# Kernel tuning notes

Measured on AMD Instinct MI355X. Metric: run time of the kernel, lower is better.

The kernel has to match this reference:

```python
import jax, jax.numpy as jnp
import numpy as np

D_IN = 1024
D_OUT = 1024
SEQ = 2048
BATCH = 4


def setup_inputs() -> dict:
    key = jax.random.key(0)
    kx, kq, kk, kv = jax.random.split(key, 4)
    x = jax.random.normal(kx, (BATCH, SEQ, D_IN), dtype=jnp.float32)
    s = 1.0 / np.sqrt(D_IN)
    Wq = jax.random.uniform(kq, (D_IN, D_OUT), dtype=jnp.float32, minval=-s, maxval=s)
    Wk = jax.random.uniform(kk, (D_IN, D_OUT), dtype=jnp.float32, minval=-s, maxval=s)
    Wv = jax.random.uniform(kv, (D_IN, D_OUT), dtype=jnp.float32, minval=-s, maxval=s)
    return {"x": x, "Wq": Wq, "Wk": Wk, "Wv": Wv}


def reference(x, Wq, Wk, Wv):
    d_k = Wq.shape[1]
    q = jnp.einsum('bsd,de->bse', x, Wq)
    k = jnp.einsum('bsd,de->bse', x, Wk)
    v = jnp.einsum('bsd,de->bse', x, Wv)
    # [B, S, S] raw scores
    scores = jnp.einsum('bqe,bke->bqk', q, k)
    S = scores.shape[-1]
    causal = jnp.triu(jnp.ones((S, S), dtype=bool), k=1)  # True above diagonal
    scores = jnp.where(causal, -jnp.inf, scores)
    attn = jax.nn.softmax(scores * (d_k ** -0.5), axis=-1)
    # dropout p=0.0 -> identity
    return jnp.einsum('bqk,bke->bqe', attn, v)
```

## Files before the change

kernel.cpp:

```cpp
#include <hip/hip_runtime.h>
#include <hip/hip_bf16.h>

typedef unsigned short u16;
typedef __bf16 bfx8 __attribute__((ext_vector_type(8)));
typedef float fx4 __attribute__((ext_vector_type(4)));

#define SEQ 2048
#define DIM 1024
#define NBATCH 4
#define SCALE 0.03125f
#define NEL ((size_t)NBATCH * SEQ * DIM)

__device__ inline u16 f2bf(float f) {
    __bf16 h = (__bf16)f;
    return __builtin_bit_cast(unsigned short, h);
}

#define GLL(gp, lp) __builtin_amdgcn_global_load_lds( \
    (const __attribute__((address_space(1))) unsigned int*)(gp), \
    (__attribute__((address_space(3))) unsigned int*)(lp), 16, 0, 0)

__global__ __launch_bounds__(256) void prep(
    const float* __restrict__ X,
    const float* __restrict__ Wq, const float* __restrict__ Wk,
    const float* __restrict__ Wv,
    u16* __restrict__ XB, u16* __restrict__ WB, u16* __restrict__ WTv,
    float* __restrict__ Lrow)
{
    __shared__ u16 t[32][33];
    int bid = blockIdx.x;
    int tid = threadIdx.x;
    if (bid < 8192) {
        size_t i = (size_t)bid * 256 + tid;
        float4 v = ((const float4*)X)[i];
        uint2 pk;
        pk.x = (unsigned)f2bf(v.x) | ((unsigned)f2bf(v.y) << 16);
        pk.y = (unsigned)f2bf(v.z) | ((unsigned)f2bf(v.w) << 16);
        ((uint2*)XB)[i] = pk;
    } else if (bid < 10240) {
        int b2 = bid - 8192;
        const float* W = (b2 < 1024) ? Wq : Wk;
        u16* out = WB + (size_t)(b2 >> 10) * 1024 * 1024;
        size_t i = (size_t)(b2 & 1023) * 256 + tid;
        float4 v = ((const float4*)W)[i];
        uint2 pk;
        pk.x = (unsigned)f2bf(v.x) | ((unsigned)f2bf(v.y) << 16);
        pk.y = (unsigned)f2bf(v.z) | ((unsigned)f2bf(v.w) << 16);
        ((uint2*)out)[i] = pk;
    } else if (bid < 11264) {
        int t2 = bid - 10240;
        int n0 = (t2 & 31) * 32, k0 = (t2 >> 5) * 32;
        int tx = tid & 31, ty = tid >> 5;
        #pragma unroll
        for (int i = 0; i < 32; i += 8)
            t[ty + i][tx] = f2bf(Wv[(size_t)(k0 + ty + i) * 1024 + n0 + tx]);
        __syncthreads();
        #pragma unroll
        for (int i = 0; i < 32; i += 8)
            WTv[(size_t)(n0 + ty + i) * 1024 + k0 + tx] = t[tx][ty + i];
    } else {
        int i = (bid - 11264) * 256 + tid;
        Lrow[i] = 0.0f;
    }
}

__global__ __launch_bounds__(256) void gemm_m(
    const u16* __restrict__ WBk, const u16* __restrict__ WBq, u16* __restrict__ MT)
{
    int m0 = blockIdx.y * 128, n0 = blockIdx.x * 128;
    __shared__ __align__(16) u16 As[128 * 32];
    __shared__ __align__(16) u16 Bs[128 * 32];
    int tid = threadIdx.x, lane = tid & 63, w = tid >> 6;
    int wm = w >> 1, wn = w & 1, lo = lane & 15, qd = lane >> 4;
    fx4 acc[4][4] = {};

    int c0 = tid, c1 = tid + 256;
    const u16* a0 = WBk + (size_t)(m0 + (c0 >> 2)) * 1024 + (((c0 & 3) ^ ((c0 >> 2) & 3)) * 8);
    const u16* a1 = WBk + (size_t)(m0 + (c1 >> 2)) * 1024 + (((c1 & 3) ^ ((c1 >> 2) & 3)) * 8);
    const u16* b0 = WBq + (size_t)(n0 + (c0 >> 2)) * 1024 + (((c0 & 3) ^ ((c0 >> 2) & 3)) * 8);
    const u16* b1 = WBq + (size_t)(n0 + (c1 >> 2)) * 1024 + (((c1 & 3) ^ ((c1 >> 2) & 3)) * 8);

    int sw = (qd ^ (lo & 3)) * 8;
    for (int k0 = 0; k0 < 1024; k0 += 32) {
        GLL(a0 + k0, &As[(size_t)c0 * 8]);
        GLL(a1 + k0, &As[(size_t)c1 * 8]);
        GLL(b0 + k0, &Bs[(size_t)c0 * 8]);
        GLL(b1 + k0, &Bs[(size_t)c1 * 8]);
        __syncthreads();
        bfx8 af[4], bf[4];
        #pragma unroll
        for (int i = 0; i < 4; i++)
            af[i] = *(const bfx8*)(&As[(wm * 64 + i * 16 + lo) * 32 + sw]);
        #pragma unroll
        for (int j = 0; j < 4; j++)
            bf[j] = *(const bfx8*)(&Bs[(wn * 64 + j * 16 + lo) * 32 + sw]);
        #pragma unroll
        for (int i = 0; i < 4; i++)
            #pragma unroll
            for (int j = 0; j < 4; j++)
                acc[i][j] = __builtin_amdgcn_mfma_f32_16x16x32_bf16(af[i], bf[j], acc[i][j], 0, 0, 0);
        __syncthreads();
    }
    #pragma unroll
    for (int i = 0; i < 4; i++)
        #pragma unroll
        for (int j = 0; j < 4; j++)
            #pragma unroll
            for (int r = 0; r < 4; r++)
                MT[(size_t)(m0 + wm * 64 + i * 16 + qd * 4 + r) * 1024
                   + n0 + wn * 64 + j * 16 + lo] = f2bf(acc[i][j][r]);
}

__global__ __launch_bounds__(256) void gemm_fast(
    const u16* __restrict__ XB, const u16* __restrict__ MT,
    const u16* __restrict__ WTv,
    u16* __restrict__ Yo, u16* __restrict__ VTo)
{
    const u16* Wz = (blockIdx.z == 0) ? MT : WTv;
    int m0 = blockIdx.y * 128, n0 = blockIdx.x * 128;

    __shared__ __align__(16) u16 As[128 * 32];
    __shared__ __align__(16) u16 Bs[128 * 32];
    __shared__ __align__(16) u16 Ct[64][132];

    int tid = threadIdx.x, lane = tid & 63, w = tid >> 6;
    int wm = w >> 1, wn = w & 1, lo = lane & 15, qd = lane >> 4;

    fx4 acc[4][4] = {};

    int c0 = tid, c1 = tid + 256;
    const u16* a0 = XB + (size_t)(m0 + (c0 >> 2)) * 1024 + (((c0 & 3) ^ ((c0 >> 2) & 3)) * 8);
    const u16* a1 = XB + (size_t)(m0 + (c1 >> 2)) * 1024 + (((c1 & 3) ^ ((c1 >> 2) & 3)) * 8);
    const u16* b0 = Wz + (size_t)(n0 + (c0 >> 2)) * 1024 + (((c0 & 3) ^ ((c0 >> 2) & 3)) * 8);
    const u16* b1 = Wz + (size_t)(n0 + (c1 >> 2)) * 1024 + (((c1 & 3) ^ ((c1 >> 2) & 3)) * 8);

    int sw = (qd ^ (lo & 3)) * 8;
    for (int k0 = 0; k0 < 1024; k0 += 32) {
        GLL(a0 + k0, &As[(size_t)c0 * 8]);
        GLL(a1 + k0, &As[(size_t)c1 * 8]);
        GLL(b0 + k0, &Bs[(size_t)c0 * 8]);
        GLL(b1 + k0, &Bs[(size_t)c1 * 8]);
        __syncthreads();

        bfx8 af[4], bf[4];
        #pragma unroll
        for (int i = 0; i < 4; i++)
            af[i] = *(const bfx8*)(&As[(wm * 64 + i * 16 + lo) * 32 + sw]);
        #pragma unroll
        for (int j = 0; j < 4; j++)
            bf[j] = *(const bfx8*)(&Bs[(wn * 64 + j * 16 + lo) * 32 + sw]);
        #pragma unroll
        for (int i = 0; i < 4; i++)
            #pragma unroll
            for (int j = 0; j < 4; j++)
                acc[i][j] = __builtin_amdgcn_mfma_f32_16x16x32_bf16(af[i], bf[j], acc[i][j], 0, 0, 0);
        __syncthreads();
    }

    if (blockIdx.z == 0) {
        #pragma unroll
        for (int i = 0; i < 4; i++)
            #pragma unroll
            for (int j = 0; j < 4; j++)
                #pragma unroll
                for (int r = 0; r < 4; r++) {
                    int row = m0 + wm * 64 + i * 16 + qd * 4 + r;
                    int col = n0 + wn * 64 + j * 16 + lo;
                    Yo[(size_t)row * 1024 + col] = f2bf(acc[i][j][r]);
                }
    } else {
        #pragma unroll
        for (int half = 0; half < 2; half++) {
            __syncthreads();
            if (wm == half) {
                #pragma unroll
                for (int i = 0; i < 4; i++)
                    #pragma unroll
                    for (int j = 0; j < 4; j++)
                        #pragma unroll
                        for (int r = 0; r < 4; r++)
                            Ct[i * 16 + qd * 4 + r][wn * 64 + j * 16 + lo] = f2bf(acc[i][j][r]);
            }
            __syncthreads();
            #pragma unroll
            for (int e = tid; e < 64 * 128; e += 256) {
                int d = e >> 6, sl = e & 63;
                int gr = m0 + half * 64 + sl;
                int bb = gr >> 11, s = gr & 2047;
                VTo[((size_t)bb * DIM + (n0 + d)) * SEQ + s] = Ct[sl][d];
            }
        }
    }
}

__global__ __launch_bounds__(512) void sgemm_exp(
    const u16* __restrict__ Y, const u16* __restrict__ XB,
    u16* __restrict__ P, float* __restrict__ Lrow)
{
    int b = blockIdx.y;
    int t = blockIdx.x;
    int i = (int)((sqrtf(8.0f * t + 1.0f) - 1.0f) * 0.5f);
    while ((i + 1) * (i + 2) / 2 <= t) i++;
    while (i * (i + 1) / 2 > t) i--;
    int j = t - i * (i + 1) / 2;

    const u16* Yb = Y + (size_t)b * SEQ * DIM;
    const u16* Xb = XB + (size_t)b * SEQ * DIM;
    u16* Pb = P + (size_t)b * SEQ * SEQ;
    float* Lb = Lrow + (size_t)b * SEQ;

    int m0 = i * 128, n0 = j * 128;

    __shared__ __align__(16) u16 As[128 * 64];
    __shared__ __align__(16) u16 Bs[128 * 64];

    int tid = threadIdx.x, lane = tid & 63, w = tid >> 6;
    int wm = w >> 2, wn = w & 3, lo = lane & 15, qd = lane >> 4;

    fx4 acc[4][2] = {};

    int c0 = tid, c1 = tid + 512;
    const u16* a0 = Yb + (size_t)(m0 + (c0 >> 3)) * 1024 + (((c0 & 7) ^ ((c0 >> 3) & 7)) * 8);
    const u16* a1 = Yb + (size_t)(m0 + (c1 >> 3)) * 1024 + (((c1 & 7) ^ ((c1 >> 3) & 7)) * 8);
    const u16* b0 = Xb + (size_t)(n0 + (c0 >> 3)) * 1024 + (((c0 & 7) ^ ((c0 >> 3) & 7)) * 8);
    const u16* b1 = Xb + (size_t)(n0 + (c1 >> 3)) * 1024 + (((c1 & 7) ^ ((c1 >> 3) & 7)) * 8);

    for (int k0 = 0; k0 < 1024; k0 += 64) {
        GLL(a0 + k0, &As[(size_t)c0 * 8]);
        GLL(a1 + k0, &As[(size_t)c1 * 8]);
        GLL(b0 + k0, &Bs[(size_t)c0 * 8]);
        GLL(b1 + k0, &Bs[(size_t)c1 * 8]);
        __syncthreads();

        #pragma unroll
        for (int kc = 0; kc < 2; kc++) {
            int sw = ((kc * 4 + qd) ^ (lo & 7)) * 8;
            bfx8 af[4], bf[2];
            #pragma unroll
            for (int ii = 0; ii < 4; ii++)
                af[ii] = *(const bfx8*)(&As[(wm * 64 + ii * 16 + lo) * 64 + sw]);
            #pragma unroll
            for (int jn = 0; jn < 2; jn++)
                bf[jn] = *(const bfx8*)(&Bs[(wn * 32 + jn * 16 + lo) * 64 + sw]);
            #pragma unroll
            for (int ii = 0; ii < 4; ii++)
                #pragma unroll
                for (int jn = 0; jn < 2; jn++)
                    acc[ii][jn] = __builtin_amdgcn_mfma_f32_16x16x32_bf16(af[ii], bf[jn], acc[ii][jn], 0, 0, 0);
        }
        __syncthreads();
    }

    #pragma unroll
    for (int ii = 0; ii < 4; ii++)
        #pragma unroll
        for (int r = 0; r < 4; r++) {
            int row = m0 + wm * 64 + ii * 16 + qd * 4 + r;
            float rs = 0.0f;
            #pragma unroll
            for (int jn = 0; jn < 2; jn++) {
                int col = n0 + wn * 32 + jn * 16 + lo;
                float s = acc[ii][jn][r] * SCALE;
                s = fminf(fmaxf(s, -30.0f), 30.0f);
                float p = (col > row) ? 0.0f : __expf(s);
                Pb[(size_t)row * SEQ + col] = f2bf(p);
                rs += p;
            }
            #pragma unroll
            for (int off = 1; off < 16; off <<= 1) rs += __shfl_xor(rs, off);
            if (lo == 0) atomicAdd(&Lb[row], rs);
        }
}

__global__ __launch_bounds__(512) void pvgemm(
    const u16* __restrict__ P, const u16* __restrict__ VT,
    const float* __restrict__ Lrow, float* __restrict__ O)
{
    int b = blockIdx.y;
    int qb = 15 - (int)(blockIdx.x >> 3);
    int db = blockIdx.x & 7;
    int m0 = qb * 128, n0 = db * 128;
    int kext = (qb + 1) * 128;

    const u16* Pb = P + (size_t)b * SEQ * SEQ;
    const u16* Vb = VT + (size_t)b * DIM * SEQ;
    const float* Lb = Lrow + (size_t)b * SEQ;
    float* Ob = O + (size_t)b * SEQ * DIM;

    __shared__ __align__(16) u16 As[128 * 64];
    __shared__ __align__(16) u16 Bs[128 * 64];

    int tid = threadIdx.x, lane = tid & 63, w = tid >> 6;
    int wm = w >> 2, wn = w & 3, lo = lane & 15, qd = lane >> 4;

    fx4 acc[4][2] = {};

    int c0 = tid, c1 = tid + 512;
    const u16* a0 = Pb + (size_t)(m0 + (c0 >> 3)) * SEQ + (((c0 & 7) ^ ((c0 >> 3) & 7)) * 8);
    const u16* a1 = Pb + (size_t)(m0 + (c1 >> 3)) * SEQ + (((c1 & 7) ^ ((c1 >> 3) & 7)) * 8);
    const u16* b0 = Vb + (size_t)(n0 + (c0 >> 3)) * SEQ + (((c0 & 7) ^ ((c0 >> 3) & 7)) * 8);
    const u16* b1 = Vb + (size_t)(n0 + (c1 >> 3)) * SEQ + (((c1 & 7) ^ ((c1 >> 3) & 7)) * 8);

    for (int k0 = 0; k0 < kext; k0 += 64) {
        GLL(a0 + k0, &As[(size_t)c0 * 8]);
        GLL(a1 + k0, &As[(size_t)c1 * 8]);
        GLL(b0 + k0, &Bs[(size_t)c0 * 8]);
        GLL(b1 + k0, &Bs[(size_t)c1 * 8]);
        __syncthreads();

        #pragma unroll
        for (int kc = 0; kc < 2; kc++) {
            int sw = ((kc * 4 + qd) ^ (lo & 7)) * 8;
            bfx8 af[4], bf[2];
            #pragma unroll
            for (int ii = 0; ii < 4; ii++)
                af[ii] = *(const bfx8*)(&As[(wm * 64 + ii * 16 + lo) * 64 + sw]);
            #pragma unroll
            for (int jn = 0; jn < 2; jn++)
                bf[jn] = *(const bfx8*)(&Bs[(wn * 32 + jn * 16 + lo) * 64 + sw]);
            #pragma unroll
            for (int ii = 0; ii < 4; ii++)
                #pragma unroll
                for (int jn = 0; jn < 2; jn++)
                    acc[ii][jn] = __builtin_amdgcn_mfma_f32_16x16x32_bf16(af[ii], bf[jn], acc[ii][jn], 0, 0, 0);
        }
        __syncthreads();
    }

    #pragma unroll
    for (int ii = 0; ii < 4; ii++)
        #pragma unroll
        for (int r = 0; r < 4; r++) {
            int row = m0 + wm * 64 + ii * 16 + qd * 4 + r;
            float linv = 1.0f / Lb[row];
            #pragma unroll
            for (int jn = 0; jn < 2; jn++) {
                int col = n0 + wn * 32 + jn * 16 + lo;
                Ob[(size_t)row * DIM + col] = acc[ii][jn][r] * linv;
            }
        }
}

__global__ __launch_bounds__(256) void gemm_legacy(
    const float* __restrict__ X,
    const float* __restrict__ Wq, const float* __restrict__ Wk, const float* __restrict__ Wv,
    u16* __restrict__ Qo, u16* __restrict__ Ko, u16* __restrict__ VTo)
{
    const int K = 1024, N = 1024;
    const float* W = (blockIdx.z == 0) ? Wq : (blockIdx.z == 1) ? Wk : Wv;
    int m0 = blockIdx.y * 128, n0 = blockIdx.x * 128;
    __shared__ __align__(16) u16 As[128 * 40];
    __shared__ __align__(16) u16 Bs[128 * 40];
    __shared__ __align__(16) u16 Ct[64][132];
    int tid = threadIdx.x, lane = tid & 63, w = tid >> 6;
    int wm = w >> 1, wn = w & 1, lo = lane & 15, qd = lane >> 4;
    fx4 acc[4][4] = {};
    for (int k0 = 0; k0 < K; k0 += 32) {
        #pragma unroll
        for (int c = tid; c < 1024; c += 256) {
            int row = c >> 3, cc = (c & 7) * 4;
            float4 v = *(const float4*)(X + (size_t)(m0 + row) * K + k0 + cc);
            uint2 pk;
            pk.x = (unsigned)f2bf(v.x) | ((unsigned)f2bf(v.y) << 16);
            pk.y = (unsigned)f2bf(v.z) | ((unsigned)f2bf(v.w) << 16);
            *(uint2*)(&As[row * 40 + cc]) = pk;
        }
        #pragma unroll
        for (int c = tid; c < 1024; c += 256) {
            int r = c >> 5, cc = (c & 31) * 4;
            float4 v = *(const float4*)(W + (size_t)(k0 + r) * N + n0 + cc);
            Bs[(cc + 0) * 40 + r] = f2bf(v.x);
            Bs[(cc + 1) * 40 + r] = f2bf(v.y);
            Bs[(cc + 2) * 40 + r] = f2bf(v.z);
            Bs[(cc + 3) * 40 + r] = f2bf(v.w);
        }
        __syncthreads();
        bfx8 af[4], bf[4];
        #pragma unroll
        for (int i = 0; i < 4; i++)
            af[i] = *(const bfx8*)(&As[(wm * 64 + i * 16 + lo) * 40 + qd * 8]);
        #pragma unroll
        for (int j = 0; j < 4; j++)
            bf[j] = *(const bfx8*)(&Bs[(wn * 64 + j * 16 + lo) * 40 + qd * 8]);
        #pragma unroll
        for (int i = 0; i < 4; i++)
            #pragma unroll
            for (int j = 0; j < 4; j++)
                acc[i][j] = __builtin_amdgcn_mfma_f32_16x16x32_bf16(af[i], bf[j], acc[i][j], 0, 0, 0);
        __syncthreads();
    }
    if (blockIdx.z != 2) {
        u16* C = (blockIdx.z == 0) ? Qo : Ko;
        #pragma unroll
        for (int i = 0; i < 4; i++)
            #pragma unroll
            for (int j = 0; j < 4; j++)
                #pragma unroll
                for (int r = 0; r < 4; r++) {
                    int row = m0 + wm * 64 + i * 16 + qd * 4 + r;
                    int col = n0 + wn * 64 + j * 16 + lo;
                    C[(size_t)row * N + col] = f2bf(acc[i][j][r]);
                }
    } else {
        #pragma unroll
        for (int half = 0; half < 2; half++) {
            __syncthreads();
            if (wm == half) {
                #pragma unroll
                for (int i = 0; i < 4; i++)
                    #pragma unroll
                    for (int j = 0; j < 4; j++)
                        #pragma unroll
                        for (int r = 0; r < 4; r++)
                            Ct[i * 16 + qd * 4 + r][wn * 64 + j * 16 + lo] = f2bf(acc[i][j][r]);
            }
            __syncthreads();
            #pragma unroll
            for (int e = tid; e < 64 * 128; e += 256) {
                int d = e >> 6, sl = e & 63;
                int gr = m0 + half * 64 + sl;
                int bb = gr >> 11, s = gr & 2047;
                VTo[((size_t)bb * DIM + (n0 + d)) * SEQ + s] = Ct[sl][d];
            }
        }
    }
}

__global__ __launch_bounds__(512) void flash_attn(
    const u16* __restrict__ Q, const u16* __restrict__ Kmat,
    const u16* __restrict__ VT, float* __restrict__ O)
{
    int b = blockIdx.y;
    int qt = (int)(gridDim.x - 1) - (int)blockIdx.x;
    int q0 = qt * 32;
    int tid = threadIdx.x;
    int lane = tid & 63, w = tid >> 6;
    int lo = lane & 15, qd = lane >> 4;

    __shared__ __align__(16) float Sp[8][32][33];
    __shared__ __align__(16) __bf16 Pl[32][40];
    __shared__ float ml[32], ll[32], al[32];

    const u16* Qb = Q + (size_t)b * SEQ * DIM;
    const u16* Kb = Kmat + (size_t)b * SEQ * DIM;
    const u16* VTb = VT + (size_t)b * DIM * SEQ;

    bfx8 qf[2][4];
    #pragma unroll
    for (int i = 0; i < 2; i++)
        #pragma unroll
        for (int c = 0; c < 4; c++)
            qf[i][c] = *(const bfx8*)(Qb + (size_t)(q0 + i * 16 + lo) * DIM + w * 128 + c * 32 + qd * 8);

    fx4 oacc[2][8] = {};
    if (tid < 32) { ml[tid] = -INFINITY; ll[tid] = 0.0f; }
    __syncthreads();

    for (int kt = 0; kt <= qt; kt++) {
        int k0 = kt * 32;
        fx4 sp[2][2] = {};
        #pragma unroll
        for (int c = 0; c < 4; c++) {
            bfx8 kf[2];
            #pragma unroll
            for (int jn = 0; jn < 2; jn++)
                kf[jn] = *(const bfx8*)(Kb + (size_t)(k0 + jn * 16 + lo) * DIM + w * 128 + c * 32 + qd * 8);
            #pragma unroll
            for (int i = 0; i < 2; i++)
                #pragma unroll
                for (int jn = 0; jn < 2; jn++)
                    sp[i][jn] = __builtin_amdgcn_mfma_f32_16x16x32_bf16(qf[i][c], kf[jn], sp[i][jn], 0, 0, 0);
        }
        #pragma unroll
        for (int i = 0; i < 2; i++)
            #pragma unroll
            for (int jn = 0; jn < 2; jn++)
                #pragma unroll
                for (int r = 0; r < 4; r++)
                    Sp[w][i * 16 + qd * 4 + r][jn * 16 + lo] = sp[i][jn][r];
        __syncthreads();
        {
            int r = tid >> 4, ci = tid & 15;
            int q = q0 + r;
            float s0 = 0.0f, s1 = 0.0f;
            #pragma unroll
            for (int p = 0; p < 8; p++) { s0 += Sp[p][r][ci]; s1 += Sp[p][r][ci + 16]; }
            s0 = fminf(fmaxf(s0 * SCALE, -1e30f), 1e30f);
            s1 = fminf(fmaxf(s1 * SCALE, -1e30f), 1e30f);
            if (k0 + ci > q)      s0 = -INFINITY;
            if (k0 + ci + 16 > q) s1 = -INFINITY;
            float mx = fmaxf(s0, s1);
            #pragma unroll
            for (int off = 1; off < 16; off <<= 1) mx = fmaxf(mx, __shfl_xor(mx, off));
            float mo = ml[r];
            float mn = fmaxf(mo, mx);
            float p0 = __expf(s0 - mn), p1 = __expf(s1 - mn);
            Pl[r][ci] = (__bf16)p0;
            Pl[r][ci + 16] = (__bf16)p1;
            float ps = p0 + p1;
            #pragma unroll
            for (int off = 1; off < 16; off <<= 1) ps += __shfl_xor(ps, off);
            if (ci == 0) {
                float alpha = __expf(mo - mn);
                ll[r] = alpha * ll[r] + ps;
                ml[r] = mn;
                al[r] = alpha;
            }
        }
        __syncthreads();
        float alocal[2][4];
        #pragma unroll
        for (int i = 0; i < 2; i++)
            #pragma unroll
            for (int r = 0; r < 4; r++)
                alocal[i][r] = al[i * 16 + qd * 4 + r];
        #pragma unroll
        for (int i = 0; i < 2; i++)
            #pragma unroll
            for (int j = 0; j < 8; j++)
                #pragma unroll
                for (int r = 0; r < 4; r++)
                    oacc[i][j][r] *= alocal[i][r];
        bfx8 pf[2];
        #pragma unroll
        for (int i = 0; i < 2; i++)
            pf[i] = *(const bfx8*)(&Pl[i * 16 + lo][qd * 8]);
        #pragma unroll
        for (int j = 0; j < 8; j++) {
            bfx8 vf = *(const bfx8*)(VTb + (size_t)(w * 128 + j * 16 + lo) * SEQ + k0 + qd * 8);
            #pragma unroll
            for (int i = 0; i < 2; i++)
                oacc[i][j] = __builtin_amdgcn_mfma_f32_16x16x32_bf16(pf[i], vf, oacc[i][j], 0, 0, 0);
        }
    }

    float linv[2][4];
    #pragma unroll
    for (int i = 0; i < 2; i++)
        #pragma unroll
        for (int r = 0; r < 4; r++)
            linv[i][r] = 1.0f / ll[i * 16 + qd * 4 + r];
    float* Ob = O + (size_t)b * SEQ * DIM;
    #pragma unroll
    for (int i = 0; i < 2; i++)
        #pragma unroll
        for (int j = 0; j < 8; j++)
            #pragma unroll
            for (int r = 0; r < 4; r++) {
                int row = q0 + i * 16 + qd * 4 + r;
                int col = w * 128 + j * 16 + lo;
                Ob[(size_t)row * DIM + col] = oacc[i][j][r] * linv[i][r];
            }
}

extern "C" void kernel_launch(void* const* d_in, const int* in_sizes, int n_in,
                              void* d_out, int out_size, void* d_ws, size_t ws_size,
                              hipStream_t stream) {
    const float* x  = (const float*)d_in[0];
    const float* Wq = (const float*)d_in[1];
    const float* Wk = (const float*)d_in[2];
    const float* Wv = (const float*)d_in[3];

    u16* ws = (u16*)d_ws;
    u16* Yp  = ws;
    u16* VTp = ws + NEL;
    u16* XBp = ws + 2 * NEL;
    u16* WBp = ws + 3 * NEL;
    u16* WTv = WBp + (size_t)2 * 1024 * 1024;
    u16* MTp = WTv + (size_t)1024 * 1024;
    u16* Pm  = MTp + (size_t)1024 * 1024;
    float* Lrow = (float*)(Pm + (size_t)NBATCH * SEQ * SEQ);

    size_t need_mat = ((size_t)3 * NEL + (size_t)4 * 1024 * 1024
                     + (size_t)NBATCH * SEQ * SEQ) * 2
                     + (size_t)NBATCH * SEQ * 4 + 1024;

    if (ws_size >= need_mat) {
        prep<<<dim3(11296), 256, 0, stream>>>(x, Wq, Wk, Wv, XBp, WBp, WTv, Lrow);
        gemm_m<<<dim3(8, 8), 256, 0, stream>>>(
            WBp + (size_t)1024 * 1024 , WBp , MTp);
        gemm_fast<<<dim3(8, 64, 2), 256, 0, stream>>>(XBp, MTp, WTv, Yp, VTp);
        sgemm_exp<<<dim3(136, NBATCH), 512, 0, stream>>>(Yp, XBp, Pm, Lrow);
        pvgemm<<<dim3(128, NBATCH), 512, 0, stream>>>(Pm, VTp, Lrow, (float*)d_out);
    } else {
        u16* Qp = ws; u16* Kp = ws + NEL; u16* VTf = ws + 2 * NEL;
        gemm_legacy<<<dim3(8, 64, 3), 256, 0, stream>>>(x, Wq, Wk, Wv, Qp, Kp, VTf);
        flash_attn<<<dim3(SEQ / 32, NBATCH), 512, 0, stream>>>(
            Qp, Kp, VTf, (float*)d_out);
    }
}
```

Baseline: 247.5 us.

## Replace 128x128 projection GEMM with double-buffered 256x256 tile kernel

The Y/V projection GEMM moves from 128x128 tiles with 256 threads and a single LDS buffer to 256x256 tiles with 512 threads and K=64 steps. Global-to-LDS loads are double-buffered with explicit vmcnt waits, and MFMA phases use s_setprio so loads overlap compute. The V transpose epilogue now writes packed 32-bit pairs. The aim is more data reuse per tile and hidden load latency, at the cost of 128KB of LDS per block, more registers and fewer blocks (256 total) across the CUs.

```diff
diff --git a/kernel.cpp b/kernel.cpp
--- a/kernel.cpp
+++ b/kernel.cpp
@@ -111,70 +111,134 @@
                    + n0 + wn * 64 + j * 16 + lo] = f2bf(acc[i][j][r]);
 }
 
-__global__ __launch_bounds__(256) void gemm_fast(
+__global__ __launch_bounds__(512) void gemm256(
     const u16* __restrict__ XB, const u16* __restrict__ MT,
     const u16* __restrict__ WTv,
     u16* __restrict__ Yo, u16* __restrict__ VTo)
 {
-    const u16* Wz = (blockIdx.z == 0) ? MT : WTv;
-    int m0 = blockIdx.y * 128, n0 = blockIdx.x * 128;
-
-    __shared__ __align__(16) u16 As[128 * 32];
-    __shared__ __align__(16) u16 Bs[128 * 32];
-    __shared__ __align__(16) u16 Ct[64][132];
-
-    int tid = threadIdx.x, lane = tid & 63, w = tid >> 6;
-    int wm = w >> 1, wn = w & 1, lo = lane & 15, qd = lane >> 4;
-
-    fx4 acc[4][4] = {};
-
-    int c0 = tid, c1 = tid + 256;
-    const u16* a0 = XB + (size_t)(m0 + (c0 >> 2)) * 1024 + (((c0 & 3) ^ ((c0 >> 2) & 3)) * 8);
-    const u16* a1 = XB + (size_t)(m0 + (c1 >> 2)) * 1024 + (((c1 & 3) ^ ((c1 >> 2) & 3)) * 8);
-    const u16* b0 = Wz + (size_t)(n0 + (c0 >> 2)) * 1024 + (((c0 & 3) ^ ((c0 >> 2) & 3)) * 8);
-    const u16* b1 = Wz + (size_t)(n0 + (c1 >> 2)) * 1024 + (((c1 & 3) ^ ((c1 >> 2) & 3)) * 8);
-
-    int sw = (qd ^ (lo & 3)) * 8;
-    for (int k0 = 0; k0 < 1024; k0 += 32) {
-        GLL(a0 + k0, &As[(size_t)c0 * 8]);
-        GLL(a1 + k0, &As[(size_t)c1 * 8]);
-        GLL(b0 + k0, &Bs[(size_t)c0 * 8]);
-        GLL(b1 + k0, &Bs[(size_t)c1 * 8]);
-        __syncthreads();
-
-        bfx8 af[4], bf[4];
-        #pragma unroll
-        for (int i = 0; i < 4; i++)
-            af[i] = *(const bfx8*)(&As[(wm * 64 + i * 16 + lo) * 32 + sw]);
-        #pragma unroll
-        for (int j = 0; j < 4; j++)
-            bf[j] = *(const bfx8*)(&Bs[(wn * 64 + j * 16 + lo) * 32 + sw]);
-        #pragma unroll
-        for (int i = 0; i < 4; i++)
+    const u16* Bop = (blockIdx.z == 0) ? MT : WTv;
+    const int m0 = blockIdx.y * 256, n0 = blockIdx.x * 256;
+
+    __shared__ __align__(16) u16 SM[65536];
+
+    const int tid = threadIdx.x, lane = tid & 63, w = tid >> 6;
+    const int wm = w >> 2, wn = w & 3, lo = lane & 15, qd = lane >> 4;
+    const int swl = lo & 7;
+
+    fx4 acc[8][4] = {};
+
+    const u16* sA[4]; const u16* sB[4]; int dofs[4];
+    #pragma unroll
+    for (int p = 0; p < 4; ++p) {
+        int n = p * 512 + tid;
+        int row = n >> 3;
+        int c = (n & 7) ^ (row & 7);
+        sA[p] = XB  + (size_t)(m0 + row) * 1024 + c * 8;
+        sB[p] = Bop + (size_t)(n0 + row) * 1024 + c * 8;
+        dofs[p] = n * 8;
+    }
+
+    auto stage = [&](int kt2) {
+        const int bb = (kt2 & 1) * 16384;
+        #pragma unroll
+        for (int p = 0; p < 4; ++p) GLL(sA[p] + kt2 * 64, &SM[bb + dofs[p]]);
+        #pragma unroll
+        for (int p = 0; p < 4; ++p) GLL(sB[p] + kt2 * 64, &SM[32768 + bb + dofs[p]]);
+    };
+
+    stage(0);
+    stage(1);
+    asm volatile("s_waitcnt vmcnt(8)" ::: "memory");
+    __builtin_amdgcn_s_barrier();
+    asm volatile("" ::: "memory");
+
+    bfx8 af[4][2], bfA[2][2], bfB[2][2];
+
+    for (int kt = 0; kt < 16; ++kt) {
+        const u16* Ab = SM + (kt & 1) * 16384;
+        const u16* Bb = SM + 32768 + (kt & 1) * 16384;
+
+        #pragma unroll
+        for (int ph = 0; ph < 4; ++ph) {
+            const int mh = ph >> 1, nh = ph & 1;
+            if (nh == 0) {
+                #pragma unroll
+                for (int ii = 0; ii < 4; ++ii)
+                    #pragma unroll
+                    for (int ks = 0; ks < 2; ++ks)
+                        af[ii][ks] = *(const bfx8*)(Ab
+                            + (wm * 128 + (mh * 4 + ii) * 16 + lo) * 64
+                            + ((ks * 4 + qd) ^ swl) * 8);
+            }
+            if (ph == 0) {
+                #pragma unroll
+                for (int jn = 0; jn < 2; ++jn)
+                    #pragma unroll
+                    for (int ks = 0; ks < 2; ++ks)
+                        bfA[jn][ks] = *(const bfx8*)(Bb
+                            + (wn * 64 + jn * 16 + lo) * 64
+                            + ((ks * 4 + qd) ^ swl) * 8);
+            }
+            if (ph == 1) {
+                #pragma unroll
+                for (int jn = 0; jn < 2; ++jn)
+                    #pragma unroll
+                    for (int ks = 0; ks < 2; ++ks)
+                        bfB[jn][ks] = *(const bfx8*)(Bb
+                            + (wn * 64 + (2 + jn) * 16 + lo) * 64
+                            + ((ks * 4 + qd) ^ swl) * 8);
+            }
+            __builtin_amdgcn_s_barrier();
+            asm volatile("s_waitcnt lgkmcnt(0)" ::: "memory");
+            __builtin_amdgcn_sched_barrier(0);
+            __builtin_amdgcn_s_setprio(1);
+            #pragma unroll
+            for (int ii = 0; ii < 4; ++ii)
+                #pragma unroll
+                for (int jn = 0; jn < 2; ++jn)
+                    #pragma unroll
+                    for (int ks = 0; ks < 2; ++ks) {
+                        if (nh == 0)
+                            acc[mh * 4 + ii][jn] = __builtin_amdgcn_mfma_f32_16x16x32_bf16(
+                                af[ii][ks], bfA[jn][ks], acc[mh * 4 + ii][jn], 0, 0, 0);
+                        else
+                            acc[mh * 4 + ii][2 + jn] = __builtin_amdgcn_mfma_f32_16x16x32_bf16(
+                                af[ii][ks], bfB[jn][ks], acc[mh * 4 + ii][2 + jn], 0, 0, 0);
+                    }
+            __builtin_amdgcn_s_setprio(0);
+            __builtin_amdgcn_s_barrier();
+            asm volatile("" ::: "memory");
+        }
+        if (kt < 14) stage(kt + 2);
+        if (kt < 15) {
+            if (kt < 14) asm volatile("s_waitcnt vmcnt(8)" ::: "memory");
+            else         asm volatile("s_waitcnt vmcnt(0)" ::: "memory");
+            __builtin_amdgcn_s_barrier();
+            asm volatile("" ::: "memory");
+        }
+    }
+
+    if (blockIdx.z == 0) {
+        #pragma unroll
+        for (int i = 0; i < 8; i++)
             #pragma unroll
             for (int j = 0; j < 4; j++)
-                acc[i][j] = __builtin_amdgcn_mfma_f32_16x16x32_bf16(af[i], bf[j], acc[i][j], 0, 0, 0);
-        __syncthreads();
-    }
-
-    if (blockIdx.z == 0) {
-        #pragma unroll
-        for (int i = 0; i < 4; i++)
-            #pragma unroll
-            for (int j = 0; j < 4; j++)
                 #pragma unroll
                 for (int r = 0; r < 4; r++) {
-                    int row = m0 + wm * 64 + i * 16 + qd * 4 + r;
+                    int row = m0 + wm * 128 + i * 16 + qd * 4 + r;
                     int col = n0 + wn * 64 + j * 16 + lo;
                     Yo[(size_t)row * 1024 + col] = f2bf(acc[i][j][r]);
                 }
     } else {
-        #pragma unroll
-        for (int half = 0; half < 2; half++) {
+        u16 (*Ct)[258] = (u16(*)[258])SM;
+        const int bb = m0 >> 11;
+        const int sbase = m0 & 2047;
+        #pragma unroll
+        for (int half = 0; half < 2; ++half) {
             __syncthreads();
             if (wm == half) {
                 #pragma unroll
-                for (int i = 0; i < 4; i++)
+                for (int i = 0; i < 8; i++)
                     #pragma unroll
                     for (int j = 0; j < 4; j++)
                         #pragma unroll
@@ -182,12 +246,11 @@
                             Ct[i * 16 + qd * 4 + r][wn * 64 + j * 16 + lo] = f2bf(acc[i][j][r]);
             }
             __syncthreads();
-            #pragma unroll
-            for (int e = tid; e < 64 * 128; e += 256) {
-                int d = e >> 6, sl = e & 63;
-                int gr = m0 + half * 64 + sl;
-                int bb = gr >> 11, s = gr & 2047;
-                VTo[((size_t)bb * DIM + (n0 + d)) * SEQ + s] = Ct[sl][d];
+            for (int e = tid; e < 16384; e += 512) {
+                int d = e >> 6, s2 = (e & 63) * 2;
+                unsigned pk = (unsigned)Ct[s2][d] | ((unsigned)Ct[s2 + 1][d] << 16);
+                *(unsigned*)&VTo[((size_t)bb * DIM + (n0 + d)) * SEQ
+                                 + sbase + half * 128 + s2] = pk;
             }
         }
     }
@@ -579,7 +642,7 @@
         prep<<<dim3(11296), 256, 0, stream>>>(x, Wq, Wk, Wv, XBp, WBp, WTv, Lrow);
         gemm_m<<<dim3(8, 8), 256, 0, stream>>>(
             WBp + (size_t)1024 * 1024 , WBp , MTp);
-        gemm_fast<<<dim3(8, 64, 2), 256, 0, stream>>>(XBp, MTp, WTv, Yp, VTp);
+        gemm256<<<dim3(4, 32, 2), 512, 0, stream>>>(XBp, MTp, WTv, Yp, VTp);
         sgemm_exp<<<dim3(136, NBATCH), 512, 0, stream>>>(Yp, XBp, Pm, Lrow);
         pvgemm<<<dim3(128, NBATCH), 512, 0, stream>>>(Pm, VTp, Lrow, (float*)d_out);
     } else {
```

Result: faster. 233.1 us (-5.8%).
